# Optimization experiments

Measured on AMD Instinct MI355X. Metric: run time of the kernel, lower is better.

Reference implementation:

```python
import jax, jax.numpy as jnp
import numpy as np

SIZE = 48
DIST = 6
PAD = DIST // 2
DESIZE = SIZE - 4  # 44
CONVEY = 0.9
RATE = 5
BATCH = 4
FLAT = DESIZE * SIZE * SIZE  # 101376


def setup_inputs() -> dict:
    key = jax.random.key(0)
    ks = jax.random.split(key, 6)
    D, H, W = DESIZE, SIZE, SIZE
    return {
        "vinput": jax.random.normal(ks[0], (BATCH, D, H, W), jnp.float32),
        "frame": jax.random.normal(ks[1], (D, H, W), jnp.float32) * 0.1,
        # 0.05 scale keeps the 216-term recurrent sums ~unit magnitude over RATE steps
        "synapse": jax.random.normal(ks[2], (D, H, W, DIST, DIST, DIST), jnp.float32) * 0.05,
        "W1": jax.random.normal(ks[3], (FLAT, 1024), jnp.float32) * 0.01,
        "b1": jnp.zeros((1024,), jnp.float32),
        "W2": jax.random.normal(ks[4], (1024, 128), jnp.float32) * 0.05,
        "b2": jnp.zeros((128,), jnp.float32),
        "W3": jax.random.normal(ks[5], (128, 10), jnp.float32) * 0.1,
        "b3": jnp.zeros((10,), jnp.float32),
    }


def _local_step(neu, syn_flat, d, p):
    """Locally-connected (unshared-weight) 3D window reduce.
    neu: (B, D, H, W); syn_flat: (D, H, W, d^3).
    For each voxel, weighted sum over its d x d x d padded neighborhood."""
    B, D, H, W = neu.shape
    pad = jnp.pad(neu, ((0, 0), (p, p), (p, p), (p, p)))
    # patches: (B, d^3, D', H', W') with valid windows; keep the first D/H/W starts
    patches = jax.lax.conv_general_dilated_patches(
        pad[:, None], filter_shape=(d, d, d), window_strides=(1, 1, 1), padding="VALID"
    )
    patches = patches[:, :, :D, :H, :W]
    return jnp.einsum("bcijk,ijkc->bijk", patches, syn_flat)


def reference(vinput, frame, synapse, W1, b1, W2, b2, W3, b3):
    D, H, W = frame.shape
    d = synapse.shape[-1]
    p = d // 2
    syn_flat = synapse.reshape(D, H, W, d * d * d)
    neu = vinput + frame  # frame broadcast over batch
    for _ in range(RATE):
        out = _local_step(neu, syn_flat, d, p)
        neu = jax.nn.relu(out) * CONVEY
    x = neu.reshape(neu.shape[0], -1)
    x = jax.nn.relu(x @ W1 + b1)
    x = jax.nn.relu(x @ W2 + b2)
    return x @ W3 + b3
```

## Files before the change

kernel.cpp:

```cpp
#include <hip/hip_runtime.h>

#define SIZE   48
#define DESIZE 44
#define PAD    3
#define BATCH  4
#define FLAT   (DESIZE*SIZE*SIZE)
#define CVOL   216

#define TJ 4
#define TK 16
#define NA 6
#define NB (TJ+5)
#define NC (TK+5)
#define NEU_T (NA*NB*NC)

#define KSLICE  96
#define NSLICES (FLAT/KSLICE)

template <int CBASE, int CNT>
__device__ __forceinline__ void do_chunk4(const float4* __restrict__ rp,
                                          const float4* __restrict__ neu4,
                                          int lanebase, float acc[4]) {
    float4 sr[CNT];
#pragma unroll
    for (int s = 0; s < CNT; ++s) sr[s] = rp[CBASE + s];
#pragma unroll
    for (int s = 0; s < CNT; ++s) {
#pragma unroll
        for (int j = 0; j < 4; ++j) {
            const int c  = (CBASE + s) * 4 + j;
            const int fd = c / 36;
            const int fh = (c % 36) / 6;
            const int fw = c % 6;
            const int off = fd * (NB * NC) + fh * NC + fw;
            const float wv = (&sr[s].x)[j];
            const float4 n4 = neu4[lanebase + off];
            acc[0] += wv * n4.x;
            acc[1] += wv * n4.y;
            acc[2] += wv * n4.z;
            acc[3] += wv * n4.w;
        }
    }
}

template <bool FIRST>
__global__ __launch_bounds__(256, 4) void k_step(const float* __restrict__ nin,
                                                 const float* __restrict__ vin,
                                                 const float* __restrict__ frame,
                                                 const float* __restrict__ syn,
                                                 float* __restrict__ nout) {
    __shared__ float4 neu4[NEU_T];
    __shared__ float  part[4 * 256];
    int t  = threadIdx.x;
    int r  = blockIdx.x;
    int i0 = r / 36;
    int r2 = r % 36;
    int j0 = (r2 / 3) * TJ;
    int k0 = (r2 % 3) * TK;

    for (int e = t; e < NEU_T; e += 256) {
        int a   = e / (NB * NC);
        int rem = e % (NB * NC);
        int jj  = rem / NC;
        int cc  = rem % NC;
        int gi = i0 + a - PAD;
        int gj = j0 + jj - PAD;
        int gk = k0 + cc - PAD;
        float4 vv = make_float4(0.f, 0.f, 0.f, 0.f);
        if ((unsigned)gi < DESIZE && (unsigned)gj < SIZE && (unsigned)gk < SIZE) {
            int idx = (gi * SIZE + gj) * SIZE + gk;
            if (FIRST) {
                float fr = frame[idx];
                vv.x = vin[0 * FLAT + idx] + fr;
                vv.y = vin[1 * FLAT + idx] + fr;
                vv.z = vin[2 * FLAT + idx] + fr;
                vv.w = vin[3 * FLAT + idx] + fr;
            } else {
                vv.x = nin[0 * FLAT + idx];
                vv.y = nin[1 * FLAT + idx];
                vv.z = nin[2 * FLAT + idx];
                vv.w = nin[3 * FLAT + idx];
            }
        }
        neu4[e] = vv;
    }
    __syncthreads();

    int w = t >> 6, l = t & 63;
    int dj = l >> 4, dk = l & 15;
    int lanebase = dj * NC + dk;
    const float4* rp = (const float4*)(syn +
        (size_t)((i0 * SIZE + j0 + dj) * SIZE + k0 + dk) * CVOL);

    float acc[4] = {0.f, 0.f, 0.f, 0.f};
    switch (w) {
        case 0:  do_chunk4< 0, 14>(rp, neu4, lanebase, acc); break;
        case 1:  do_chunk4<14, 14>(rp, neu4, lanebase, acc); break;
        case 2:  do_chunk4<28, 13>(rp, neu4, lanebase, acc); break;
        default: do_chunk4<41, 13>(rp, neu4, lanebase, acc); break;
    }
#pragma unroll
    for (int bb = 0; bb < 4; ++bb) part[bb * 256 + t] = acc[bb];
    __syncthreads();

    {
        int bb = t >> 6, lv = t & 63;
        float s = part[bb * 256 + lv] + part[bb * 256 + 64 + lv] +
                  part[bb * 256 + 128 + lv] + part[bb * 256 + 192 + lv];
        s = fmaxf(s, 0.f) * 0.9f;
        int dj2 = lv >> 4, dk2 = lv & 15;
        nout[(size_t)bb * FLAT + (i0 * SIZE + (j0 + dj2)) * SIZE + (k0 + dk2)] = s;
    }
}

__global__ __launch_bounds__(256) void k_mlp1(const float* __restrict__ xc,
                                              const float* __restrict__ W1,
                                              float* __restrict__ partial) {
    __shared__ float xs[KSLICE * 4];
    int t = threadIdx.x;
    int s = blockIdx.x;
    int k0 = s * KSLICE;
    for (int e = t; e < KSLICE * 4; e += 256) {
        int kk = e >> 2, b = e & 3;
        xs[e] = xc[(size_t)b * FLAT + k0 + kk];
    }
    __syncthreads();
    float acc[4][4] = {};
    const float* wp = W1 + (size_t)k0 * 1024 + t * 4;
#pragma unroll 8
    for (int kk = 0; kk < KSLICE; ++kk) {
        float4 w  = *(const float4*)(wp + (size_t)kk * 1024);
        float4 xv = *(const float4*)(xs + kk * 4);
        acc[0][0] += xv.x * w.x; acc[0][1] += xv.x * w.y; acc[0][2] += xv.x * w.z; acc[0][3] += xv.x * w.w;
        acc[1][0] += xv.y * w.x; acc[1][1] += xv.y * w.y; acc[1][2] += xv.y * w.z; acc[1][3] += xv.y * w.w;
        acc[2][0] += xv.z * w.x; acc[2][1] += xv.z * w.y; acc[2][2] += xv.z * w.z; acc[2][3] += xv.z * w.w;
        acc[3][0] += xv.w * w.x; acc[3][1] += xv.w * w.y; acc[3][2] += xv.w * w.z; acc[3][3] += xv.w * w.w;
    }
#pragma unroll
    for (int b = 0; b < 4; ++b) {
        float4 o = make_float4(acc[b][0], acc[b][1], acc[b][2], acc[b][3]);
        *(float4*)(partial + (size_t)s * 4096 + b * 1024 + t * 4) = o;
    }
}

__global__ __launch_bounds__(256) void k_reduce1(const float* __restrict__ partial,
                                                 const float* __restrict__ b1,
                                                 float* __restrict__ h1) {
    __shared__ float red[16][17];
    int t = threadIdx.x;
    int e0 = blockIdx.x * 16;
    int eo = t & 15, sl = t >> 4;
    float acc = 0.f;
    for (int it = 0; it < NSLICES / 16; ++it) {
        int s = sl + 16 * it;
        acc += partial[(size_t)s * 4096 + e0 + eo];
    }
    red[sl][eo] = acc;
    __syncthreads();
    if (t < 16) {
        float a = 0.f;
#pragma unroll
        for (int rr = 0; rr < 16; ++rr) a += red[rr][t];
        int e = e0 + t;
        h1[e] = fmaxf(a + b1[e & 1023], 0.f);
    }
}

__global__ __launch_bounds__(64) void k_mlp2(const float* __restrict__ h1,
                                             const float* __restrict__ W2,
                                             float* __restrict__ partial2) {
    __shared__ float xs[32 * 4];
    int t = threadIdx.x;
    int bid = blockIdx.x;
    int s = bid >> 1, ch = bid & 1;
    int k0 = s * 32;
    for (int e = t; e < 128; e += 64) {
        int kk = e >> 2, b = e & 3;
        xs[e] = h1[b * 1024 + k0 + kk];
    }
    __syncthreads();
    float acc[4] = {0.f, 0.f, 0.f, 0.f};
    int n2 = ch * 64 + t;
#pragma unroll
    for (int kk = 0; kk < 32; ++kk) {
        float w = W2[(size_t)(k0 + kk) * 128 + n2];
        float4 xv = *(const float4*)(xs + kk * 4);
        acc[0] += xv.x * w; acc[1] += xv.y * w; acc[2] += xv.z * w; acc[3] += xv.w * w;
    }
#pragma unroll
    for (int b = 0; b < 4; ++b) partial2[s * 512 + b * 128 + n2] = acc[b];
}

__global__ __launch_bounds__(128) void k_mlp3(const float* __restrict__ partial2,
                                              const float* __restrict__ b2,
                                              const float* __restrict__ W3,
                                              const float* __restrict__ b3,
                                              float* __restrict__ out) {
    __shared__ float h2[512];
    int t = threadIdx.x;
    for (int e = t; e < 512; e += 128) {
        int n2 = e & 127;
        float a = b2[n2];
#pragma unroll 8
        for (int s = 0; s < 32; ++s) a += partial2[s * 512 + e];
        h2[e] = fmaxf(a, 0.f);
    }
    __syncthreads();
    if (t < 40) {
        int b = t / 10, o = t % 10;
        float a = b3[o];
        for (int k = 0; k < 128; ++k) a += h2[b * 128 + k] * W3[k * 10 + o];
        out[b * 10 + o] = a;
    }
}

extern "C" void kernel_launch(void* const* d_in, const int* in_sizes, int n_in,
                              void* d_out, int out_size, void* d_ws, size_t ws_size,
                              hipStream_t stream) {
    const float* vin   = (const float*)d_in[0];
    const float* frame = (const float*)d_in[1];
    const float* syn   = (const float*)d_in[2];
    const float* W1    = (const float*)d_in[3];
    const float* b1    = (const float*)d_in[4];
    const float* W2    = (const float*)d_in[5];
    const float* b2    = (const float*)d_in[6];
    const float* W3    = (const float*)d_in[7];
    const float* b3    = (const float*)d_in[8];
    float* out = (float*)d_out;

    float* ws = (float*)d_ws;
    float* A   = ws;
    float* B   = A + (size_t)BATCH * FLAT;
    float* P1  = B + (size_t)BATCH * FLAT;
    float* H1  = P1 + (size_t)NSLICES * 4096;
    float* P2  = H1 + 4096;

    k_step<true ><<<1584, 256, 0, stream>>>(nullptr, vin, frame, syn, A);
    k_step<false><<<1584, 256, 0, stream>>>(A, nullptr, nullptr, syn, B);
    k_step<false><<<1584, 256, 0, stream>>>(B, nullptr, nullptr, syn, A);
    k_step<false><<<1584, 256, 0, stream>>>(A, nullptr, nullptr, syn, B);
    k_step<false><<<1584, 256, 0, stream>>>(B, nullptr, nullptr, syn, A);

    k_mlp1<<<NSLICES, 256, 0, stream>>>(A, W1, P1);
    k_reduce1<<<256, 256, 0, stream>>>(P1, b1, H1);
    k_mlp2<<<64, 64, 0, stream>>>(H1, W2, P2);
    k_mlp3<<<1, 128, 0, stream>>>(P2, b2, W3, b3, out);
}
```

Before: 719.7 us.

## Transpose synapse weights per tile for coalesced loads and interleave batch activations

Adds a pre-pass that rearranges the synapse tensor into a per-tile layout where consecutive lanes read consecutive float4s, so the five step kernels get coalesced weight loads instead of 864-byte strided ones. Activations are stored batch-interleaved as float4 per voxel, turning four scalar gathers into one vector load and letting the MLP input load use float4. The register-held weight chunk is split into two halves, which reduces register pressure. The cost is an extra full pass over the 80 MB synapse tensor plus an equally large workspace buffer, which must be paid back by faster reads across the five steps.

```diff
diff --git a/kernel.cpp b/kernel.cpp
--- a/kernel.cpp
+++ b/kernel.cpp
@@ -13,42 +13,78 @@
 #define NB (TJ+5)
 #define NC (TK+5)
 #define NEU_T (NA*NB*NC)
+#define NTILE 1584
+#define C4    54
 
 #define KSLICE  96
 #define NSLICES (FLAT/KSLICE)
 
+__global__ __launch_bounds__(256) void k_synT(const float* __restrict__ syn,
+                                              float* __restrict__ synT) {
+    int r  = blockIdx.x;
+    int i0 = r / 36;
+    int r2 = r % 36;
+    int j0 = (r2 / 3) * TJ;
+    int k0 = (r2 % 3) * TK;
+    int t  = threadIdx.x;
+    float4* dst = (float4*)synT + (size_t)r * (C4 * 64);
+    for (int e = t; e < C4 * 64; e += 256) {
+        int c4 = e >> 6, l = e & 63;
+        int dj = l >> 4, dk = l & 15;
+        const float4* src = (const float4*)(syn +
+            (size_t)((i0 * SIZE + j0 + dj) * SIZE + k0 + dk) * CVOL);
+        dst[e] = src[c4];
+    }
+}
+
 template <int CBASE, int CNT>
-__device__ __forceinline__ void do_chunk4(const float4* __restrict__ rp,
+__device__ __forceinline__ void do_chunk4(const float4* __restrict__ sp,
                                           const float4* __restrict__ neu4,
                                           int lanebase, float acc[4]) {
-    float4 sr[CNT];
-#pragma unroll
-    for (int s = 0; s < CNT; ++s) sr[s] = rp[CBASE + s];
-#pragma unroll
-    for (int s = 0; s < CNT; ++s) {
-#pragma unroll
-        for (int j = 0; j < 4; ++j) {
-            const int c  = (CBASE + s) * 4 + j;
-            const int fd = c / 36;
-            const int fh = (c % 36) / 6;
-            const int fw = c % 6;
-            const int off = fd * (NB * NC) + fh * NC + fw;
-            const float wv = (&sr[s].x)[j];
-            const float4 n4 = neu4[lanebase + off];
-            acc[0] += wv * n4.x;
-            acc[1] += wv * n4.y;
-            acc[2] += wv * n4.z;
-            acc[3] += wv * n4.w;
+    constexpr int H1n = (CNT + 1) / 2;
+    constexpr int H2n = CNT - H1n;
+    {
+        float4 sr[H1n];
+#pragma unroll
+        for (int s = 0; s < H1n; ++s) sr[s] = sp[(CBASE + s) * 64];
+#pragma unroll
+        for (int s = 0; s < H1n; ++s) {
+#pragma unroll
+            for (int j = 0; j < 4; ++j) {
+                const int c  = (CBASE + s) * 4 + j;
+                const int off = (c / 36) * (NB * NC) + ((c % 36) / 6) * NC + (c % 6);
+                const float wv = (&sr[s].x)[j];
+                const float4 n4 = neu4[lanebase + off];
+                acc[0] += wv * n4.x; acc[1] += wv * n4.y;
+                acc[2] += wv * n4.z; acc[3] += wv * n4.w;
+            }
         }
     }
+    {
+        float4 sr[H2n];
+#pragma unroll
+        for (int s = 0; s < H2n; ++s) sr[s] = sp[(CBASE + H1n + s) * 64];
+#pragma unroll
+        for (int s = 0; s < H2n; ++s) {
+#pragma unroll
+            for (int j = 0; j < 4; ++j) {
+                const int c  = (CBASE + H1n + s) * 4 + j;
+                const int off = (c / 36) * (NB * NC) + ((c % 36) / 6) * NC + (c % 6);
+                const float wv = (&sr[s].x)[j];
+                const float4 n4 = neu4[lanebase + off];
+                acc[0] += wv * n4.x; acc[1] += wv * n4.y;
+                acc[2] += wv * n4.z; acc[3] += wv * n4.w;
+            }
+        }
+    }
 }
 
 template <bool FIRST>
-__global__ __launch_bounds__(256, 4) void k_step(const float* __restrict__ nin,
+__global__ __launch_bounds__(256, 4) void k_step(const float4* __restrict__ nin4,
                                                  const float* __restrict__ vin,
                                                  const float* __restrict__ frame,
-                                                 const float* __restrict__ syn,
-                                                 float* __restrict__ nout) {
+                                                 const float* __restrict__ synT,
+                                                 float4* __restrict__ nout4) {
     __shared__ float4 neu4[NEU_T];
     __shared__ float  part[4 * 256];
     int t  = threadIdx.x;
@@ -76,10 +112,7 @@
                 vv.z = vin[2 * FLAT + idx] + fr;
                 vv.w = vin[3 * FLAT + idx] + fr;
             } else {
-                vv.x = nin[0 * FLAT + idx];
-                vv.y = nin[1 * FLAT + idx];
-                vv.z = nin[2 * FLAT + idx];
-                vv.w = nin[3 * FLAT + idx];
+                vv = nin4[idx];
             }
         }
         neu4[e] = vv;
@@ -89,41 +122,43 @@
     int w = t >> 6, l = t & 63;
     int dj = l >> 4, dk = l & 15;
     int lanebase = dj * NC + dk;
-    const float4* rp = (const float4*)(syn +
-        (size_t)((i0 * SIZE + j0 + dj) * SIZE + k0 + dk) * CVOL);
+    const float4* sp = (const float4*)synT + (size_t)r * (C4 * 64) + l;
 
     float acc[4] = {0.f, 0.f, 0.f, 0.f};
     switch (w) {
-        case 0:  do_chunk4< 0, 14>(rp, neu4, lanebase, acc); break;
-        case 1:  do_chunk4<14, 14>(rp, neu4, lanebase, acc); break;
-        case 2:  do_chunk4<28, 13>(rp, neu4, lanebase, acc); break;
-        default: do_chunk4<41, 13>(rp, neu4, lanebase, acc); break;
+        case 0:  do_chunk4< 0, 14>(sp, neu4, lanebase, acc); break;
+        case 1:  do_chunk4<14, 14>(sp, neu4, lanebase, acc); break;
+        case 2:  do_chunk4<28, 13>(sp, neu4, lanebase, acc); break;
+        default: do_chunk4<41, 13>(sp, neu4, lanebase, acc); break;
     }
 #pragma unroll
     for (int bb = 0; bb < 4; ++bb) part[bb * 256 + t] = acc[bb];
     __syncthreads();
 
-    {
-        int bb = t >> 6, lv = t & 63;
-        float s = part[bb * 256 + lv] + part[bb * 256 + 64 + lv] +
-                  part[bb * 256 + 128 + lv] + part[bb * 256 + 192 + lv];
-        s = fmaxf(s, 0.f) * 0.9f;
-        int dj2 = lv >> 4, dk2 = lv & 15;
-        nout[(size_t)bb * FLAT + (i0 * SIZE + (j0 + dj2)) * SIZE + (k0 + dk2)] = s;
-    }
-}
-
-__global__ __launch_bounds__(256) void k_mlp1(const float* __restrict__ xc,
+    if (t < 64) {
+        float4 o;
+        o.x = part[0 * 256 + t] + part[0 * 256 + 64 + t] + part[0 * 256 + 128 + t] + part[0 * 256 + 192 + t];
+        o.y = part[1 * 256 + t] + part[1 * 256 + 64 + t] + part[1 * 256 + 128 + t] + part[1 * 256 + 192 + t];
+        o.z = part[2 * 256 + t] + part[2 * 256 + 64 + t] + part[2 * 256 + 128 + t] + part[2 * 256 + 192 + t];
+        o.w = part[3 * 256 + t] + part[3 * 256 + 64 + t] + part[3 * 256 + 128 + t] + part[3 * 256 + 192 + t];
+        o.x = fmaxf(o.x, 0.f) * 0.9f;
+        o.y = fmaxf(o.y, 0.f) * 0.9f;
+        o.z = fmaxf(o.z, 0.f) * 0.9f;
+        o.w = fmaxf(o.w, 0.f) * 0.9f;
+        int dj2 = t >> 4, dk2 = t & 15;
+        nout4[(i0 * SIZE + (j0 + dj2)) * SIZE + (k0 + dk2)] = o;
+    }
+}
+
+__global__ __launch_bounds__(256) void k_mlp1(const float4* __restrict__ x4,
                                               const float* __restrict__ W1,
                                               float* __restrict__ partial) {
     __shared__ float xs[KSLICE * 4];
     int t = threadIdx.x;
     int s = blockIdx.x;
     int k0 = s * KSLICE;
-    for (int e = t; e < KSLICE * 4; e += 256) {
-        int kk = e >> 2, b = e & 3;
-        xs[e] = xc[(size_t)b * FLAT + k0 + kk];
-    }
+    for (int e = t; e < KSLICE; e += 256)
+        ((float4*)xs)[e] = x4[k0 + e];
     __syncthreads();
     float acc[4][4] = {};
     const float* wp = W1 + (size_t)k0 * 1024 + t * 4;
@@ -234,14 +269,17 @@
     float* P1  = B + (size_t)BATCH * FLAT;
     float* H1  = P1 + (size_t)NSLICES * 4096;
     float* P2  = H1 + 4096;
-
-    k_step<true ><<<1584, 256, 0, stream>>>(nullptr, vin, frame, syn, A);
-    k_step<false><<<1584, 256, 0, stream>>>(A, nullptr, nullptr, syn, B);
-    k_step<false><<<1584, 256, 0, stream>>>(B, nullptr, nullptr, syn, A);
-    k_step<false><<<1584, 256, 0, stream>>>(A, nullptr, nullptr, syn, B);
-    k_step<false><<<1584, 256, 0, stream>>>(B, nullptr, nullptr, syn, A);
-
-    k_mlp1<<<NSLICES, 256, 0, stream>>>(A, W1, P1);
+    float* ST  = P2 + 16384;
+
+    k_synT<<<NTILE, 256, 0, stream>>>(syn, ST);
+
+    k_step<true ><<<NTILE, 256, 0, stream>>>(nullptr, vin, frame, ST, (float4*)A);
+    k_step<false><<<NTILE, 256, 0, stream>>>((const float4*)A, nullptr, nullptr, ST, (float4*)B);
+    k_step<false><<<NTILE, 256, 0, stream>>>((const float4*)B, nullptr, nullptr, ST, (float4*)A);
+    k_step<false><<<NTILE, 256, 0, stream>>>((const float4*)A, nullptr, nullptr, ST, (float4*)B);
+    k_step<false><<<NTILE, 256, 0, stream>>>((const float4*)B, nullptr, nullptr, ST, (float4*)A);
+
+    k_mlp1<<<NSLICES, 256, 0, stream>>>((const float4*)A, W1, P1);
     k_reduce1<<<256, 256, 0, stream>>>(P1, b1, H1);
     k_mlp2<<<64, 64, 0, stream>>>(H1, W2, P2);
     k_mlp3<<<1, 128, 0, stream>>>(P2, b2, W3, b3, out);
```

Result: no change. 728.4 us (+1.2%).
